# Performance work log

Measured on AMD Instinct MI355X. Metric: run time of the kernel, lower is better.

## Reference

```python
import jax, jax.numpy as jnp
import numpy as np

N_POIS = 100000
N_HYPEREDGES = 50000
NNZ = 1600000
D = 256
NUM_LAYERS = 2
P_DROP = 0.3


def setup_inputs() -> dict:
    key = jax.random.key(0)
    ks = jax.random.split(key, 10)
    scale = 1.0 / (1.0 - P_DROP)
    drop1 = jax.random.bernoulli(ks[4], 1.0 - P_DROP, (NUM_LAYERS, N_POIS, D)).astype(jnp.float32) * scale
    drop2 = jax.random.bernoulli(ks[5], 1.0 - P_DROP, (NUM_LAYERS, N_POIS, D)).astype(jnp.float32) * scale
    return {
        "pois_embs": jax.random.normal(ks[0], (N_POIS, D), dtype=jnp.float32),
        "tar_vals": jax.random.uniform(ks[1], (NNZ,), dtype=jnp.float32),
        "src_vals": jax.random.uniform(ks[2], (NNZ,), dtype=jnp.float32),
        "layer_attention": jnp.ones((NUM_LAYERS + 1,), dtype=jnp.float32),
        "drop1": drop1,
        "drop2": drop2,
        "tar_rows": jax.random.randint(ks[6], (NNZ,), 0, N_HYPEREDGES, dtype=jnp.int32),
        "tar_cols": jax.random.randint(ks[7], (NNZ,), 0, N_POIS, dtype=jnp.int32),
        "src_rows": jax.random.randint(ks[8], (NNZ,), 0, N_POIS, dtype=jnp.int32),
        "src_cols": jax.random.randint(ks[9], (NNZ,), 0, N_HYPEREDGES, dtype=jnp.int32),
    }


def _spmm(rows, cols, vals, dense, num_rows):
    # COO sparse @ dense: gather rows of `dense` by cols, scale, scatter-add by rows
    return jax.ops.segment_sum(vals[:, None] * dense[cols], rows, num_segments=num_rows)


def reference(pois_embs, tar_vals, src_vals, layer_attention, drop1, drop2,
              tar_rows, tar_cols, src_rows, src_cols):
    embs = pois_embs
    layer_outs = [embs]
    for i in range(NUM_LAYERS):
        # msg_tar = HG_poi_tar @ embs  -> [n_hyperedges, d]
        msg_tar = _spmm(tar_rows, tar_cols, tar_vals, embs, N_HYPEREDGES)
        # msg_src = HG_poi_src @ msg_tar -> [n_pois, d]
        msg_src = _spmm(src_rows, src_cols, src_vals, msg_tar, N_POIS)
        msg_src = jax.nn.relu(msg_src) * drop1[i]      # conv-layer dropout
        embs = (msg_src + layer_outs[-1]) * drop2[i]   # residual + F.dropout
        layer_outs.append(embs)
    w = jax.nn.softmax(layer_attention)                # [num_layers+1]
    stacked = jnp.stack(layer_outs)                    # [L+1, n_pois, d]
    return jnp.sum(stacked * w[:, None, None], axis=0)
```

## Files before the change

### kernel.cpp

```cpp
#include <hip/hip_runtime.h>

#define NPOIS 100000
#define NHYP  50000
#define NNZE  1600000
#define DIM   256

#define SH_TAR 6
#define SH_SRC 7
#define NBUCK 782
#define CHUNK 6250

typedef unsigned int uint;

#define DROP_C ((float)(1.0 / (1.0 - 0.3)))

__device__ __forceinline__ uint pack_bf16(float a, float b) {
    uint ua = __float_as_uint(a); ua += 0x7fffu + ((ua >> 16) & 1u);
    uint ub = __float_as_uint(b); ub += 0x7fffu + ((ub >> 16) & 1u);
    return (ua >> 16) | (ub & 0xffff0000u);
}
__device__ __forceinline__ float4 unpack_h(uint2 u) {
    return make_float4(__uint_as_float(u.x << 16), __uint_as_float(u.x & 0xffff0000u),
                       __uint_as_float(u.y << 16), __uint_as_float(u.y & 0xffff0000u));
}

__global__ __launch_bounds__(256) void to_h_kernel(
    const float4* __restrict__ in, uint2* __restrict__ out, int n4)
{
    int stride = gridDim.x * blockDim.x;
    for (int i = blockIdx.x * blockDim.x + threadIdx.x; i < n4; i += stride) {
        float4 x = in[i];
        out[i] = make_uint2(pack_bf16(x.x, x.y), pack_bf16(x.z, x.w));
    }
}

__global__ __launch_bounds__(256) void drop_bits_kernel(
    const float4* __restrict__ d1, const float4* __restrict__ d2,
    uint* __restrict__ o1, uint* __restrict__ o2, int nw)
{
    int t = blockIdx.x * blockDim.x + threadIdx.x;
    if (t >= 2 * nw) return;
    const float4* src = (t < nw) ? d1 : d2;
    uint* dst = (t < nw) ? o1 : o2;
    int w = (t < nw) ? t : t - nw;
    uint m = 0;
#pragma unroll
    for (int q = 0; q < 8; ++q) {
        float4 v = src[(size_t)w * 8 + q];
        m |= (v.x != 0.f ? 1u : 0u) << (4 * q);
        m |= (v.y != 0.f ? 2u : 0u) << (4 * q);
        m |= (v.z != 0.f ? 4u : 0u) << (4 * q);
        m |= (v.w != 0.f ? 8u : 0u) << (4 * q);
    }
    dst[w] = m;
}


__global__ __launch_bounds__(256) void hist_coarse(
    const int* __restrict__ tr, const int* __restrict__ sr,
    int* __restrict__ c_tar, int* __restrict__ c_src, int nnz)
{
    __shared__ int lt[NBUCK], ls[NBUCK];
    int t = threadIdx.x;
    int s = blockIdx.x * CHUNK, e = min(s + CHUNK, nnz);
    for (int i = t; i < NBUCK; i += 256) { lt[i] = 0; ls[i] = 0; }
    __syncthreads();
    for (int i = s + t; i < e; i += 256) {
        atomicAdd(&lt[tr[i] >> SH_TAR], 1);
        atomicAdd(&ls[sr[i] >> SH_SRC], 1);
    }
    __syncthreads();
    for (int i = t; i < NBUCK; i += 256) {
        if (lt[i]) atomicAdd(&c_tar[i], lt[i]);
        if (ls[i]) atomicAdd(&c_src[i], ls[i]);
    }
}

__global__ __launch_bounds__(256) void scan_offsets(
    const int* __restrict__ c_tar, const int* __restrict__ c_src,
    int* __restrict__ off_tar, int* __restrict__ tl_tar,
    int* __restrict__ off_src, int* __restrict__ tl_src)
{
    __shared__ int lds[256];
    int t = threadIdx.x;
    for (int sel = 0; sel < 2; ++sel) {
        const int* c = sel ? c_src : c_tar;
        int* off = sel ? off_src : off_tar;
        int* tl  = sel ? tl_src : tl_tar;
        int carry = 0;
        for (int base = 0; base < NBUCK; base += 256) {
            int i = base + t;
            int v = (i < NBUCK) ? c[i] : 0;
            lds[t] = v;
            __syncthreads();
            for (int o = 1; o < 256; o <<= 1) {
                int x = (t >= o) ? lds[t - o] : 0;
                __syncthreads();
                lds[t] += x;
                __syncthreads();
            }
            int excl = carry + lds[t] - v;
            if (i < NBUCK) { off[i] = excl; tl[i] = excl; }
            carry += lds[255];
            __syncthreads();
        }
        if (t == 0) off[NBUCK] = carry;
        __syncthreads();
    }
}

__global__ __launch_bounds__(256) void csr_stage(
    const int* __restrict__ tar_rows, const int* __restrict__ tar_cols,
    const float* __restrict__ tar_vals,
    const int* __restrict__ src_rows, const int* __restrict__ src_cols,
    const float* __restrict__ src_vals,
    int* __restrict__ tl_tar, uint2* __restrict__ stag_tar,
    int* __restrict__ tl_src, uint2* __restrict__ stag_src, int nnz)
{
    __shared__ int lh[NBUCK];
    __shared__ int lbase[NBUCK];
    int t = threadIdx.x;
    bool is_src = blockIdx.x >= 256;
    int blk = is_src ? blockIdx.x - 256 : blockIdx.x;
    const int* rows = is_src ? src_rows : tar_rows;
    const int* cols = is_src ? src_cols : tar_cols;
    const float* vals = is_src ? src_vals : tar_vals;
    int* tails = is_src ? tl_src : tl_tar;
    uint2* stag = is_src ? stag_src : stag_tar;
    const int SH = is_src ? SH_SRC : SH_TAR;

    int s = blk * CHUNK, e = min(s + CHUNK, nnz);
    for (int i = t; i < NBUCK; i += 256) lh[i] = 0;
    __syncthreads();
    for (int i = s + t; i < e; i += 256) atomicAdd(&lh[rows[i] >> SH], 1);
    __syncthreads();
    for (int i = t; i < NBUCK; i += 256) {
        int c = lh[i];
        lbase[i] = c ? atomicAdd(&tails[i], c) : 0;
        lh[i] = 0;
    }
    __syncthreads();
    for (int i = s + t; i < e; i += 256) {
        int r = rows[i];
        int b = r >> SH;
        int pos = lbase[b] + atomicAdd(&lh[b], 1);
        uint uv = __float_as_uint(vals[i]);
        uv += 0x7fffu + ((uv >> 16) & 1u);
        stag[pos] = make_uint2((uint)r, ((uint)cols[i] << 15) | ((uv >> 16) & 0x7fffu));
    }
}

__global__ __launch_bounds__(256) void csr_finalize(
    const uint2* __restrict__ stag_tar, const int* __restrict__ off_tar,
    int* __restrict__ rp_tar, uint* __restrict__ ep_tar,
    const uint2* __restrict__ stag_src, const int* __restrict__ off_src,
    int* __restrict__ rp_src, uint* __restrict__ ep_src, int nnz)
{
    __shared__ uint2 recs[4096];
    __shared__ int lhist[128];
    __shared__ int lbase[129];
    bool is_src = blockIdx.x >= NBUCK;
    int b = is_src ? blockIdx.x - NBUCK : blockIdx.x;
    const uint2* stag = is_src ? stag_src : stag_tar;
    const int* off = is_src ? off_src : off_tar;
    int* rp = is_src ? rp_src : rp_tar;
    uint* ep = is_src ? ep_src : ep_tar;
    const int SH = is_src ? SH_SRC : SH_TAR;
    const int RPB = 1 << SH;
    const int nrows = is_src ? NPOIS : NHYP;
    int t = threadIdx.x;
    int base = off[b];
    int n = off[b + 1] - base;
    int r0 = b << SH;

    for (int i = t; i < RPB; i += 256) lhist[i] = 0;
    __syncthreads();

    bool fit = (n <= 4096);
    for (int i = t; i < n; i += 256) {
        uint2 rec = stag[base + i];
        if (fit) recs[i] = rec;
        atomicAdd(&lhist[(int)rec.x - r0], 1);
    }
    __syncthreads();
    if (t == 0) {
        int run = 0;
        for (int i = 0; i < RPB; ++i) { lbase[i] = run; run += lhist[i]; }
        lbase[RPB] = run;
    }
    __syncthreads();
    for (int i = t; i < RPB; i += 256) {
        int rg = r0 + i;
        if (rg < nrows) rp[rg] = base + lbase[i];
    }
    if (b == 0 && t == 0) rp[nrows] = nnz;
    for (int i = t; i < RPB; i += 256) lhist[i] = 0;
    __syncthreads();
    for (int i = t; i < n; i += 256) {
        uint2 rec = fit ? recs[i] : stag[base + i];
        int rl = (int)rec.x - r0;
        int slot = lbase[rl] + atomicAdd(&lhist[rl], 1);
        ep[base + slot] = rec.y;
    }
}

#define GCH 8

__device__ __forceinline__ float4 gather_h(
    const int* __restrict__ rp, const uint* __restrict__ ep,
    const uint2* __restrict__ dh, int row, int lane)
{
    int s = rp[row], e = rp[row + 1];
    float4 acc = {0.f, 0.f, 0.f, 0.f};
    for (int k = s; k < e; k += GCH) {
        uint ev[GCH];
#pragma unroll
        for (int j = 0; j < GCH; ++j)
            ev[j] = (k + j < e) ? ep[k + j] : 0u;
        uint2 x[GCH];
#pragma unroll
        for (int j = 0; j < GCH; ++j)
            x[j] = dh[(size_t)(ev[j] >> 15) * (DIM / 4) + lane];
#pragma unroll
        for (int j = 0; j < GCH; ++j) {
            float vv = __uint_as_float((ev[j] & 0x7fffu) << 16);
            acc.x += vv * __uint_as_float(x[j].x << 16);
            acc.y += vv * __uint_as_float(x[j].x & 0xffff0000u);
            acc.z += vv * __uint_as_float(x[j].y << 16);
            acc.w += vv * __uint_as_float(x[j].y & 0xffff0000u);
        }
    }
    return acc;
}

__device__ __forceinline__ float4 gather_f(
    const int* __restrict__ rp, const uint* __restrict__ ep,
    const float4* __restrict__ d4, int row, int lane)
{
    int s = rp[row], e = rp[row + 1];
    float4 acc = {0.f, 0.f, 0.f, 0.f};
    for (int k = s; k < e; k += GCH) {
        uint ev[GCH];
#pragma unroll
        for (int j = 0; j < GCH; ++j)
            ev[j] = (k + j < e) ? ep[k + j] : 0u;
        float4 x[GCH];
#pragma unroll
        for (int j = 0; j < GCH; ++j)
            x[j] = d4[(size_t)(ev[j] >> 15) * (DIM / 4) + lane];
#pragma unroll
        for (int j = 0; j < GCH; ++j) {
            float vv = __uint_as_float((ev[j] & 0x7fffu) << 16);
            acc.x += vv * x[j].x;
            acc.y += vv * x[j].y;
            acc.z += vv * x[j].z;
            acc.w += vv * x[j].w;
        }
    }
    return acc;
}

__device__ __forceinline__ float4 drop4(const uint* __restrict__ bm, int row, int lane)
{
    uint m = bm[(size_t)row * 8 + (lane >> 3)] >> ((lane & 7) * 4);
    return make_float4((m & 1u) ? DROP_C : 0.f, (m & 2u) ? DROP_C : 0.f,
                       (m & 4u) ? DROP_C : 0.f, (m & 8u) ? DROP_C : 0.f);
}

template <bool BF16D>
__global__ __launch_bounds__(256) void spmm_to_h(
    const int* __restrict__ rp, const uint* __restrict__ ep,
    const void* __restrict__ dense, uint2* __restrict__ out_h, int nrows)
{
    int wid  = (blockIdx.x * blockDim.x + threadIdx.x) >> 6;
    int lane = threadIdx.x & 63;
    if (wid >= nrows) return;
    int row = __builtin_amdgcn_readfirstlane(wid);
    float4 a = BF16D ? gather_h(rp, ep, (const uint2*)dense, row, lane)
                     : gather_f(rp, ep, (const float4*)dense, row, lane);
    out_h[(size_t)row * (DIM / 4) + lane] = make_uint2(pack_bf16(a.x, a.y), pack_bf16(a.z, a.w));
}

template <bool PH, bool BITS>
__global__ __launch_bounds__(256) void spmm_epi1(
    const int* __restrict__ rp, const uint* __restrict__ ep,
    const uint2* __restrict__ msg_h,
    const uint2* __restrict__ pois_h, const float4* __restrict__ pois_f,
    const float4* __restrict__ d1, const float4* __restrict__ d2,
    const uint* __restrict__ bm1, const uint* __restrict__ bm2,
    uint2* __restrict__ out_h, int nrows)
{
    int wid  = (blockIdx.x * blockDim.x + threadIdx.x) >> 6;
    int lane = threadIdx.x & 63;
    if (wid >= nrows) return;
    int row = __builtin_amdgcn_readfirstlane(wid);
    size_t idx = (size_t)row * (DIM / 4) + lane;
    float4 a, b;
    if (BITS) { a = drop4(bm1, row, lane); b = drop4(bm2, row, lane); }
    else      { a = d1[idx]; b = d2[idx]; }
    float4 p = PH ? unpack_h(pois_h[idx]) : pois_f[idx];
    float4 m = gather_h(rp, ep, msg_h, row, lane);
    float4 r;
    r.x = (fmaxf(m.x, 0.f) * a.x + p.x) * b.x;
    r.y = (fmaxf(m.y, 0.f) * a.y + p.y) * b.y;
    r.z = (fmaxf(m.z, 0.f) * a.z + p.z) * b.z;
    r.w = (fmaxf(m.w, 0.f) * a.w + p.w) * b.w;
    out_h[idx] = make_uint2(pack_bf16(r.x, r.y), pack_bf16(r.z, r.w));
}

template <bool PH, bool BITS>
__global__ __launch_bounds__(256) void spmm_final(
    const int* __restrict__ rp, const uint* __restrict__ ep,
    const uint2* __restrict__ msg_h,
    const uint2* __restrict__ pois_h, const float4* __restrict__ pois_f,
    const uint2* __restrict__ embs1_h,
    const float4* __restrict__ d1, const float4* __restrict__ d2,
    const uint* __restrict__ bm1, const uint* __restrict__ bm2,
    const float* __restrict__ attn, float4* __restrict__ out, int nrows)
{
    int wid  = (blockIdx.x * blockDim.x + threadIdx.x) >> 6;
    int lane = threadIdx.x & 63;
    if (wid >= nrows) return;
    int row = __builtin_amdgcn_readfirstlane(wid);

    float a0 = attn[0], a1 = attn[1], a2 = attn[2];
    float mx = fmaxf(a0, fmaxf(a1, a2));
    float e0 = __expf(a0 - mx), e1 = __expf(a1 - mx), e2 = __expf(a2 - mx);
    float inv = 1.f / (e0 + e1 + e2);
    float w0 = e0 * inv, w1 = e1 * inv, w2 = e2 * inv;

    size_t idx = (size_t)row * (DIM / 4) + lane;
    float4 a, b;
    if (BITS) { a = drop4(bm1, row, lane); b = drop4(bm2, row, lane); }
    else      { a = d1[idx]; b = d2[idx]; }
    float4 p0 = PH ? unpack_h(pois_h[idx]) : pois_f[idx];
    float4 p1 = unpack_h(embs1_h[idx]);
    float4 m = gather_h(rp, ep, msg_h, row, lane);
    float4 r;
    r.x = w0 * p0.x + w1 * p1.x + w2 * ((fmaxf(m.x, 0.f) * a.x + p1.x) * b.x);
    r.y = w0 * p0.y + w1 * p1.y + w2 * ((fmaxf(m.y, 0.f) * a.y + p1.y) * b.y);
    r.z = w0 * p0.z + w1 * p1.z + w2 * ((fmaxf(m.z, 0.f) * a.z + p1.z) * b.z);
    r.w = w0 * p0.w + w1 * p1.w + w2 * ((fmaxf(m.w, 0.f) * a.w + p1.w) * b.w);
    out[idx] = r;
}

extern "C" void kernel_launch(void* const* d_in, const int* in_sizes, int n_in,
                              void* d_out, int out_size, void* d_ws, size_t ws_size,
                              hipStream_t stream)
{
    const float* pois     = (const float*)d_in[0];
    const float* tar_vals = (const float*)d_in[1];
    const float* src_vals = (const float*)d_in[2];
    const float* attn     = (const float*)d_in[3];
    const float* drop1    = (const float*)d_in[4];
    const float* drop2    = (const float*)d_in[5];
    const int*   tar_rows = (const int*)d_in[6];
    const int*   tar_cols = (const int*)d_in[7];
    const int*   src_rows = (const int*)d_in[8];
    const int*   src_cols = (const int*)d_in[9];
    float* out = (float*)d_out;

    const size_t ptn = (size_t)NPOIS * DIM;

    char* p = (char*)d_ws;
    uint* ep_tar   = (uint*)p;              p += (size_t)NNZE * 4;
    uint* ep_src   = (uint*)p;              p += (size_t)NNZE * 4;
    int*  rp_tar   = (int*)p;               p += 200064;
    int*  rp_src   = (int*)p;               p += 400064;
    int*  misc     = (int*)p;               p += 32768;
    uint2* msg_h   = (uint2*)p;             p += (size_t)NHYP * DIM * 2;
    uint2* embs1_h = (uint2*)p;             p += (size_t)NPOIS * DIM * 2;

    const size_t bits_words = (size_t)2 * NPOIS * 8;
    uint* bits1 = (uint*)p;
    uint* bits2 = bits1 + bits_words;       p += 2 * bits_words * 4;
    size_t bits_need = (size_t)(p - (char*)d_ws);
    bool have_bits = ws_size >= bits_need;

    uint2* pois_h  = (uint2*)p;
    bool full = ws_size >= bits_need + ptn * 2;

    int* cntc_tar = misc;
    int* off_tar  = cntc_tar + NBUCK;
    int* tl_tar   = off_tar + NBUCK + 1;
    int* cntc_src = tl_tar + NBUCK;
    int* off_src  = cntc_src + NBUCK;
    int* tl_src   = off_src + NBUCK + 1;

    uint2* stag_tar = (uint2*)msg_h;
    uint2* stag_src = stag_tar + NNZE;

    const int BLK = 256;

    if (full)
        to_h_kernel<<<(int)(ptn / 4 + BLK - 1) / BLK, BLK, 0, stream>>>(
            (const float4*)pois, pois_h, (int)(ptn / 4));

    if (have_bits) {
        int nw = (int)(2 * ptn / 32);
        drop_bits_kernel<<<(2 * nw + BLK - 1) / BLK, BLK, 0, stream>>>(
            (const float4*)drop1, (const float4*)drop2, bits1, bits2, nw);
    }

    hipMemsetAsync(misc, 0, 32768, stream);
    hist_coarse<<<256, BLK, 0, stream>>>(tar_rows, src_rows, cntc_tar, cntc_src, NNZE);
    scan_offsets<<<1, BLK, 0, stream>>>(cntc_tar, cntc_src, off_tar, tl_tar, off_src, tl_src);
    csr_stage<<<512, BLK, 0, stream>>>(
        tar_rows, tar_cols, tar_vals, src_rows, src_cols, src_vals,
        tl_tar, stag_tar, tl_src, stag_src, NNZE);
    csr_finalize<<<2 * NBUCK, BLK, 0, stream>>>(
        stag_tar, off_tar, rp_tar, ep_tar,
        stag_src, off_src, rp_src, ep_src, NNZE);

    const int gb_hyp = NHYP / 4;
    const int gb_poi = NPOIS / 4;

    const float4* d1_l0 = (const float4*)drop1;
    const float4* d2_l0 = (const float4*)drop2;
    const float4* d1_l1 = (const float4*)(drop1 + ptn);
    const float4* d2_l1 = (const float4*)(drop2 + ptn);
    const uint* b1_l0 = bits1;
    const uint* b2_l0 = bits2;
    const uint* b1_l1 = bits1 + (size_t)NPOIS * 8;
    const uint* b2_l1 = bits2 + (size_t)NPOIS * 8;

    if (full)
        spmm_to_h<true><<<gb_hyp, BLK, 0, stream>>>(rp_tar, ep_tar, pois_h, msg_h, NHYP);
    else
        spmm_to_h<false><<<gb_hyp, BLK, 0, stream>>>(rp_tar, ep_tar, pois, msg_h, NHYP);

    if (full && have_bits)
        spmm_epi1<true, true><<<gb_poi, BLK, 0, stream>>>(
            rp_src, ep_src, msg_h, pois_h, (const float4*)pois,
            d1_l0, d2_l0, b1_l0, b2_l0, embs1_h, NPOIS);
    else if (full)
        spmm_epi1<true, false><<<gb_poi, BLK, 0, stream>>>(
            rp_src, ep_src, msg_h, pois_h, (const float4*)pois,
            d1_l0, d2_l0, b1_l0, b2_l0, embs1_h, NPOIS);
    else if (have_bits)
        spmm_epi1<false, true><<<gb_poi, BLK, 0, stream>>>(
            rp_src, ep_src, msg_h, pois_h, (const float4*)pois,
            d1_l0, d2_l0, b1_l0, b2_l0, embs1_h, NPOIS);
    else
        spmm_epi1<false, false><<<gb_poi, BLK, 0, stream>>>(
            rp_src, ep_src, msg_h, pois_h, (const float4*)pois,
            d1_l0, d2_l0, b1_l0, b2_l0, embs1_h, NPOIS);

    spmm_to_h<true><<<gb_hyp, BLK, 0, stream>>>(rp_tar, ep_tar, embs1_h, msg_h, NHYP);

    if (full && have_bits)
        spmm_final<true, true><<<gb_poi, BLK, 0, stream>>>(
            rp_src, ep_src, msg_h, pois_h, (const float4*)pois, embs1_h,
            d1_l1, d2_l1, b1_l1, b2_l1, attn, (float4*)out, NPOIS);
    else if (full)
        spmm_final<true, false><<<gb_poi, BLK, 0, stream>>>(
            rp_src, ep_src, msg_h, pois_h, (const float4*)pois, embs1_h,
            d1_l1, d2_l1, b1_l1, b2_l1, attn, (float4*)out, NPOIS);
    else if (have_bits)
        spmm_final<false, true><<<gb_poi, BLK, 0, stream>>>(
            rp_src, ep_src, msg_h, pois_h, (const float4*)pois, embs1_h,
            d1_l1, d2_l1, b1_l1, b2_l1, attn, (float4*)out, NPOIS);
    else
        spmm_final<false, false><<<gb_poi, BLK, 0, stream>>>(
            rp_src, ep_src, msg_h, pois_h, (const float4*)pois, embs1_h,
            d1_l1, d2_l1, b1_l1, b2_l1, attn, (float4*)out, NPOIS);
}
```

Measured before the change: 1.184 ms.

## Fuse whole pipeline into one cooperative persistent kernel with grid syncs

Replaces the sequence of separate kernel launches (bf16 conversion, dropout bit packing, CSR build via bucketed histogram/scatter, two SpMM layers with fused epilogues) with a single cooperative persistent kernel that separates phases with grid-wide syncs. The aim is to remove per-launch overhead and gaps between kernels. In exchange, the grid is capped at occupancy times 256 blocks, and the sort phases lose the earlier per-bucket LDS record caching. Grid syncs also cost time, and serial single-block scans now stall the whole grid. The old multi-kernel path is kept as a fallback if the cooperative launch fails.

```diff
diff --git a/kernel.cpp b/kernel.cpp
--- a/kernel.cpp
+++ b/kernel.cpp
@@ -1,4 +1,7 @@
 #include <hip/hip_runtime.h>
+#include <hip/hip_cooperative_groups.h>
+
+namespace cg = cooperative_groups;
 
 #define NPOIS 100000
 #define NHYP  50000
@@ -14,6 +17,19 @@
 
 #define DROP_C ((float)(1.0 / (1.0 - 0.3)))
 
+#define OFF_EPT   0
+#define OFF_EPS   6400000
+#define OFF_RPT   12800000
+#define OFF_RPS   13000064
+#define OFF_MISC  13400128
+#define OFF_MSG   13432896
+#define OFF_EMB   39032896
+#define OFF_BITS1 90232896
+#define OFF_BITS2 96632896
+#define OFF_POISH 103032896
+#define NEED_BITS 103032896
+#define NEED_FULL 154232896
+
 __device__ __forceinline__ uint pack_bf16(float a, float b) {
     uint ua = __float_as_uint(a); ua += 0x7fffu + ((ua >> 16) & 1u);
     uint ub = __float_as_uint(b); ub += 0x7fffu + ((ub >> 16) & 1u);
@@ -22,6 +38,331 @@
 __device__ __forceinline__ float4 unpack_h(uint2 u) {
     return make_float4(__uint_as_float(u.x << 16), __uint_as_float(u.x & 0xffff0000u),
                        __uint_as_float(u.y << 16), __uint_as_float(u.y & 0xffff0000u));
+}
+
+#define GCH 8
+
+__device__ __forceinline__ float4 gather_h(
+    const int* rp, const uint* ep, const uint2* dh, int row, int lane)
+{
+    int s = rp[row], e = rp[row + 1];
+    float4 acc = {0.f, 0.f, 0.f, 0.f};
+    for (int k = s; k < e; k += GCH) {
+        uint ev[GCH];
+#pragma unroll
+        for (int j = 0; j < GCH; ++j)
+            ev[j] = (k + j < e) ? ep[k + j] : 0u;
+        uint2 x[GCH];
+#pragma unroll
+        for (int j = 0; j < GCH; ++j)
+            x[j] = dh[(size_t)(ev[j] >> 15) * (DIM / 4) + lane];
+#pragma unroll
+        for (int j = 0; j < GCH; ++j) {
+            float vv = __uint_as_float((ev[j] & 0x7fffu) << 16);
+            acc.x += vv * __uint_as_float(x[j].x << 16);
+            acc.y += vv * __uint_as_float(x[j].x & 0xffff0000u);
+            acc.z += vv * __uint_as_float(x[j].y << 16);
+            acc.w += vv * __uint_as_float(x[j].y & 0xffff0000u);
+        }
+    }
+    return acc;
+}
+
+__device__ __forceinline__ float4 gather_f(
+    const int* rp, const uint* ep, const float4* d4, int row, int lane)
+{
+    int s = rp[row], e = rp[row + 1];
+    float4 acc = {0.f, 0.f, 0.f, 0.f};
+    for (int k = s; k < e; k += GCH) {
+        uint ev[GCH];
+#pragma unroll
+        for (int j = 0; j < GCH; ++j)
+            ev[j] = (k + j < e) ? ep[k + j] : 0u;
+        float4 x[GCH];
+#pragma unroll
+        for (int j = 0; j < GCH; ++j)
+            x[j] = d4[(size_t)(ev[j] >> 15) * (DIM / 4) + lane];
+#pragma unroll
+        for (int j = 0; j < GCH; ++j) {
+            float vv = __uint_as_float((ev[j] & 0x7fffu) << 16);
+            acc.x += vv * x[j].x;
+            acc.y += vv * x[j].y;
+            acc.z += vv * x[j].z;
+            acc.w += vv * x[j].w;
+        }
+    }
+    return acc;
+}
+
+__device__ __forceinline__ float4 drop4(const uint* bm, int row, int lane)
+{
+    uint m = bm[(size_t)row * 8 + (lane >> 3)] >> ((lane & 7) * 4);
+    return make_float4((m & 1u) ? DROP_C : 0.f, (m & 2u) ? DROP_C : 0.f,
+                       (m & 4u) ? DROP_C : 0.f, (m & 8u) ? DROP_C : 0.f);
+}
+
+__global__ __launch_bounds__(256) void mega(
+    const float* pois, const float* tar_vals, const float* src_vals,
+    const float* attn, const float* drop1, const float* drop2,
+    const int* tar_rows, const int* tar_cols,
+    const int* src_rows, const int* src_cols,
+    float4* out, char* ws, int full, int have_bits)
+{
+    cg::grid_group grid = cg::this_grid();
+
+    uint*  ep_tar  = (uint*)(ws + OFF_EPT);
+    uint*  ep_src  = (uint*)(ws + OFF_EPS);
+    int*   rp_tar  = (int*)(ws + OFF_RPT);
+    int*   rp_src  = (int*)(ws + OFF_RPS);
+    int*   misc    = (int*)(ws + OFF_MISC);
+    uint2* msg_h   = (uint2*)(ws + OFF_MSG);
+    uint2* embs1_h = (uint2*)(ws + OFF_EMB);
+    uint*  bits1   = (uint*)(ws + OFF_BITS1);
+    uint*  bits2   = (uint*)(ws + OFF_BITS2);
+    uint2* pois_h  = (uint2*)(ws + OFF_POISH);
+
+    int* cntc_tar = misc;
+    int* off_tar  = cntc_tar + NBUCK;
+    int* tl_tar   = off_tar + NBUCK + 1;
+    int* cntc_src = tl_tar + NBUCK;
+    int* off_src  = cntc_src + NBUCK;
+    int* tl_src   = off_src + NBUCK + 1;
+
+    uint2* stag_tar = (uint2*)msg_h;
+    uint2* stag_src = stag_tar + NNZE;
+
+    __shared__ int lds_a[NBUCK];
+    __shared__ int lds_b[NBUCK];
+
+    const int B    = gridDim.x;
+    const int t    = threadIdx.x;
+    const int tid  = blockIdx.x * 256 + t;
+    const int nthr = B * 256;
+    const int lane = t & 63;
+    const int w0   = tid >> 6;
+    const int wstr = nthr >> 6;
+
+    for (int i = tid; i < 8192; i += nthr) misc[i] = 0;
+    if (full) {
+        const float4* pin = (const float4*)pois;
+        for (int i = tid; i < NPOIS * DIM / 4; i += nthr) {
+            float4 x = pin[i];
+            pois_h[i] = make_uint2(pack_bf16(x.x, x.y), pack_bf16(x.z, x.w));
+        }
+    }
+    if (have_bits) {
+        const float4* s1 = (const float4*)drop1;
+        const float4* s2 = (const float4*)drop2;
+        for (int w = tid; w < 1600000; w += nthr) {
+            uint m1 = 0, m2 = 0;
+#pragma unroll
+            for (int q = 0; q < 8; ++q) {
+                float4 v = s1[(size_t)w * 8 + q];
+                m1 |= (v.x != 0.f ? 1u : 0u) << (4 * q);
+                m1 |= (v.y != 0.f ? 2u : 0u) << (4 * q);
+                m1 |= (v.z != 0.f ? 4u : 0u) << (4 * q);
+                m1 |= (v.w != 0.f ? 8u : 0u) << (4 * q);
+                float4 u = s2[(size_t)w * 8 + q];
+                m2 |= (u.x != 0.f ? 1u : 0u) << (4 * q);
+                m2 |= (u.y != 0.f ? 2u : 0u) << (4 * q);
+                m2 |= (u.z != 0.f ? 4u : 0u) << (4 * q);
+                m2 |= (u.w != 0.f ? 8u : 0u) << (4 * q);
+            }
+            bits1[w] = m1; bits2[w] = m2;
+        }
+    }
+    grid.sync();
+
+    {
+        int per = (NNZE + B - 1) / B;
+        int s = blockIdx.x * per, e = min(s + per, NNZE);
+        for (int i = t; i < NBUCK; i += 256) { lds_a[i] = 0; lds_b[i] = 0; }
+        __syncthreads();
+        for (int i = s + t; i < e; i += 256) {
+            atomicAdd(&lds_a[tar_rows[i] >> SH_TAR], 1);
+            atomicAdd(&lds_b[src_rows[i] >> SH_SRC], 1);
+        }
+        __syncthreads();
+        for (int i = t; i < NBUCK; i += 256) {
+            if (lds_a[i]) atomicAdd(&cntc_tar[i], lds_a[i]);
+            if (lds_b[i]) atomicAdd(&cntc_src[i], lds_b[i]);
+        }
+    }
+    grid.sync();
+
+    if (blockIdx.x == 0) {
+        for (int sel = 0; sel < 2; ++sel) {
+            const int* c = sel ? cntc_src : cntc_tar;
+            int* off = sel ? off_src : off_tar;
+            int* tl  = sel ? tl_src : tl_tar;
+            int carry = 0;
+            for (int base = 0; base < NBUCK; base += 256) {
+                int i = base + t;
+                int v = (i < NBUCK) ? c[i] : 0;
+                lds_a[t] = v;
+                __syncthreads();
+                for (int o = 1; o < 256; o <<= 1) {
+                    int x = (t >= o) ? lds_a[t - o] : 0;
+                    __syncthreads();
+                    lds_a[t] += x;
+                    __syncthreads();
+                }
+                int excl = carry + lds_a[t] - v;
+                if (i < NBUCK) { off[i] = excl; tl[i] = excl; }
+                carry += lds_a[255];
+                __syncthreads();
+            }
+            if (t == 0) off[NBUCK] = carry;
+            __syncthreads();
+        }
+    }
+    grid.sync();
+
+    for (int c = blockIdx.x; c < 512; c += B) {
+        bool is_src = c >= 256;
+        int blk = c & 255;
+        const int* rows = is_src ? src_rows : tar_rows;
+        const int* cols = is_src ? src_cols : tar_cols;
+        const float* vals = is_src ? src_vals : tar_vals;
+        int* tails = is_src ? tl_src : tl_tar;
+        uint2* stag = is_src ? stag_src : stag_tar;
+        const int SH = is_src ? SH_SRC : SH_TAR;
+        int s = blk * CHUNK, e = min(s + CHUNK, NNZE);
+        for (int i = t; i < NBUCK; i += 256) lds_a[i] = 0;
+        __syncthreads();
+        for (int i = s + t; i < e; i += 256) atomicAdd(&lds_a[rows[i] >> SH], 1);
+        __syncthreads();
+        for (int i = t; i < NBUCK; i += 256) {
+            int cc = lds_a[i];
+            lds_b[i] = cc ? atomicAdd(&tails[i], cc) : 0;
+            lds_a[i] = 0;
+        }
+        __syncthreads();
+        for (int i = s + t; i < e; i += 256) {
+            int r = rows[i];
+            int b = r >> SH;
+            int pos = lds_b[b] + atomicAdd(&lds_a[b], 1);
+            uint uv = __float_as_uint(vals[i]);
+            uv += 0x7fffu + ((uv >> 16) & 1u);
+            stag[pos] = make_uint2((uint)r, ((uint)cols[i] << 15) | ((uv >> 16) & 0x7fffu));
+        }
+        __syncthreads();
+    }
+    grid.sync();
+
+    for (int c = blockIdx.x; c < 2 * NBUCK; c += B) {
+        bool is_src = c >= NBUCK;
+        int b = is_src ? c - NBUCK : c;
+        const uint2* stag = is_src ? stag_src : stag_tar;
+        const int* off = is_src ? off_src : off_tar;
+        int* rp = is_src ? rp_src : rp_tar;
+        uint* ep = is_src ? ep_src : ep_tar;
+        const int SH = is_src ? SH_SRC : SH_TAR;
+        const int RPB = 1 << SH;
+        const int nrows = is_src ? NPOIS : NHYP;
+        int base = off[b];
+        int n = off[b + 1] - base;
+        int r0 = b << SH;
+        for (int i = t; i < RPB; i += 256) lds_a[i] = 0;
+        __syncthreads();
+        for (int i = t; i < n; i += 256)
+            atomicAdd(&lds_a[(int)stag[base + i].x - r0], 1);
+        __syncthreads();
+        if (t == 0) {
+            int run = 0;
+            for (int i = 0; i < RPB; ++i) { lds_b[i] = run; run += lds_a[i]; }
+        }
+        __syncthreads();
+        for (int i = t; i < RPB; i += 256) {
+            int rg = r0 + i;
+            if (rg < nrows) rp[rg] = base + lds_b[i];
+        }
+        for (int i = t; i < RPB; i += 256) lds_a[i] = 0;
+        __syncthreads();
+        for (int i = t; i < n; i += 256) {
+            uint2 rec = stag[base + i];
+            int rl = (int)rec.x - r0;
+            int slot = lds_b[rl] + atomicAdd(&lds_a[rl], 1);
+            ep[base + slot] = rec.y;
+        }
+        __syncthreads();
+    }
+    if (blockIdx.x == 0 && t == 0) { rp_tar[NHYP] = NNZE; rp_src[NPOIS] = NNZE; }
+    grid.sync();
+
+    if (full) {
+        for (int r = w0; r < NHYP; r += wstr) {
+            int row = __builtin_amdgcn_readfirstlane(r);
+            float4 a = gather_h(rp_tar, ep_tar, pois_h, row, lane);
+            msg_h[(size_t)row * (DIM / 4) + lane] =
+                make_uint2(pack_bf16(a.x, a.y), pack_bf16(a.z, a.w));
+        }
+    } else {
+        for (int r = w0; r < NHYP; r += wstr) {
+            int row = __builtin_amdgcn_readfirstlane(r);
+            float4 a = gather_f(rp_tar, ep_tar, (const float4*)pois, row, lane);
+            msg_h[(size_t)row * (DIM / 4) + lane] =
+                make_uint2(pack_bf16(a.x, a.y), pack_bf16(a.z, a.w));
+        }
+    }
+    grid.sync();
+
+    {
+        const float4* d1 = (const float4*)drop1;
+        const float4* d2 = (const float4*)drop2;
+        for (int r = w0; r < NPOIS; r += wstr) {
+            int row = __builtin_amdgcn_readfirstlane(r);
+            size_t idx = (size_t)row * (DIM / 4) + lane;
+            float4 a, b;
+            if (have_bits) { a = drop4(bits1, row, lane); b = drop4(bits2, row, lane); }
+            else           { a = d1[idx]; b = d2[idx]; }
+            float4 p = full ? unpack_h(pois_h[idx]) : ((const float4*)pois)[idx];
+            float4 m = gather_h(rp_src, ep_src, msg_h, row, lane);
+            float4 o;
+            o.x = (fmaxf(m.x, 0.f) * a.x + p.x) * b.x;
+            o.y = (fmaxf(m.y, 0.f) * a.y + p.y) * b.y;
+            o.z = (fmaxf(m.z, 0.f) * a.z + p.z) * b.z;
+            o.w = (fmaxf(m.w, 0.f) * a.w + p.w) * b.w;
+            embs1_h[idx] = make_uint2(pack_bf16(o.x, o.y), pack_bf16(o.z, o.w));
+        }
+    }
+    grid.sync();
+
+    for (int r = w0; r < NHYP; r += wstr) {
+        int row = __builtin_amdgcn_readfirstlane(r);
+        float4 a = gather_h(rp_tar, ep_tar, embs1_h, row, lane);
+        msg_h[(size_t)row * (DIM / 4) + lane] =
+            make_uint2(pack_bf16(a.x, a.y), pack_bf16(a.z, a.w));
+    }
+    grid.sync();
+
+    {
+        float t0 = attn[0], t1 = attn[1], t2 = attn[2];
+        float mx = fmaxf(t0, fmaxf(t1, t2));
+        float e0 = __expf(t0 - mx), e1 = __expf(t1 - mx), e2 = __expf(t2 - mx);
+        float inv = 1.f / (e0 + e1 + e2);
+        float wt0 = e0 * inv, wt1 = e1 * inv, wt2 = e2 * inv;
+        const float4* d1 = (const float4*)(drop1 + (size_t)NPOIS * DIM);
+        const float4* d2 = (const float4*)(drop2 + (size_t)NPOIS * DIM);
+        const uint* b1 = bits1 + (size_t)NPOIS * 8;
+        const uint* b2 = bits2 + (size_t)NPOIS * 8;
+        for (int r = w0; r < NPOIS; r += wstr) {
+            int row = __builtin_amdgcn_readfirstlane(r);
+            size_t idx = (size_t)row * (DIM / 4) + lane;
+            float4 a, b;
+            if (have_bits) { a = drop4(b1, row, lane); b = drop4(b2, row, lane); }
+            else           { a = d1[idx]; b = d2[idx]; }
+            float4 p0 = full ? unpack_h(pois_h[idx]) : ((const float4*)pois)[idx];
+            float4 p1 = unpack_h(embs1_h[idx]);
+            float4 m = gather_h(rp_src, ep_src, msg_h, row, lane);
+            float4 o;
+            o.x = wt0 * p0.x + wt1 * p1.x + wt2 * ((fmaxf(m.x, 0.f) * a.x + p1.x) * b.x);
+            o.y = wt0 * p0.y + wt1 * p1.y + wt2 * ((fmaxf(m.y, 0.f) * a.y + p1.y) * b.y);
+            o.z = wt0 * p0.z + wt1 * p1.z + wt2 * ((fmaxf(m.z, 0.f) * a.z + p1.z) * b.z);
+            o.w = wt0 * p0.w + wt1 * p1.w + wt2 * ((fmaxf(m.w, 0.f) * a.w + p1.w) * b.w);
+            out[idx] = o;
+        }
+    }
 }
 
 __global__ __launch_bounds__(256) void to_h_kernel(
@@ -54,7 +395,6 @@
     }
     dst[w] = m;
 }
-
 
 __global__ __launch_bounds__(256) void hist_coarse(
     const int* __restrict__ tr, const int* __restrict__ sr,
@@ -175,7 +515,6 @@
 
     for (int i = t; i < RPB; i += 256) lhist[i] = 0;
     __syncthreads();
-
     bool fit = (n <= 4096);
     for (int i = t; i < n; i += 256) {
         uint2 rec = stag[base + i];
@@ -202,69 +541,6 @@
         int slot = lbase[rl] + atomicAdd(&lhist[rl], 1);
         ep[base + slot] = rec.y;
     }
-}
-
-#define GCH 8
-
-__device__ __forceinline__ float4 gather_h(
-    const int* __restrict__ rp, const uint* __restrict__ ep,
-    const uint2* __restrict__ dh, int row, int lane)
-{
-    int s = rp[row], e = rp[row + 1];
-    float4 acc = {0.f, 0.f, 0.f, 0.f};
-    for (int k = s; k < e; k += GCH) {
-        uint ev[GCH];
-#pragma unroll
-        for (int j = 0; j < GCH; ++j)
-            ev[j] = (k + j < e) ? ep[k + j] : 0u;
-        uint2 x[GCH];
-#pragma unroll
-        for (int j = 0; j < GCH; ++j)
-            x[j] = dh[(size_t)(ev[j] >> 15) * (DIM / 4) + lane];
-#pragma unroll
-        for (int j = 0; j < GCH; ++j) {
-            float vv = __uint_as_float((ev[j] & 0x7fffu) << 16);
-            acc.x += vv * __uint_as_float(x[j].x << 16);
-            acc.y += vv * __uint_as_float(x[j].x & 0xffff0000u);
-            acc.z += vv * __uint_as_float(x[j].y << 16);
-            acc.w += vv * __uint_as_float(x[j].y & 0xffff0000u);
-        }
-    }
-    return acc;
-}
-
-__device__ __forceinline__ float4 gather_f(
-    const int* __restrict__ rp, const uint* __restrict__ ep,
-    const float4* __restrict__ d4, int row, int lane)
-{
-    int s = rp[row], e = rp[row + 1];
-    float4 acc = {0.f, 0.f, 0.f, 0.f};
-    for (int k = s; k < e; k += GCH) {
-        uint ev[GCH];
-#pragma unroll
-        for (int j = 0; j < GCH; ++j)
-            ev[j] = (k + j < e) ? ep[k + j] : 0u;
-        float4 x[GCH];
-#pragma unroll
-        for (int j = 0; j < GCH; ++j)
-            x[j] = d4[(size_t)(ev[j] >> 15) * (DIM / 4) + lane];
-#pragma unroll
-        for (int j = 0; j < GCH; ++j) {
-            float vv = __uint_as_float((ev[j] & 0x7fffu) << 16);
-            acc.x += vv * x[j].x;
-            acc.y += vv * x[j].y;
-            acc.z += vv * x[j].z;
-            acc.w += vv * x[j].w;
-        }
-    }
-    return acc;
-}
-
-__device__ __forceinline__ float4 drop4(const uint* __restrict__ bm, int row, int lane)
-{
-    uint m = bm[(size_t)row * 8 + (lane >> 3)] >> ((lane & 7) * 4);
-    return make_float4((m & 1u) ? DROP_C : 0.f, (m & 2u) ? DROP_C : 0.f,
-                       (m & 4u) ? DROP_C : 0.f, (m & 8u) ? DROP_C : 0.f);
 }
 
 template <bool BF16D>
@@ -358,27 +634,48 @@
     const int*   tar_cols = (const int*)d_in[7];
     const int*   src_rows = (const int*)d_in[8];
     const int*   src_cols = (const int*)d_in[9];
-    float* out = (float*)d_out;
+    float4* out = (float4*)d_out;
+    char* ws = (char*)d_ws;
 
     const size_t ptn = (size_t)NPOIS * DIM;
-
-    char* p = (char*)d_ws;
-    uint* ep_tar   = (uint*)p;              p += (size_t)NNZE * 4;
-    uint* ep_src   = (uint*)p;              p += (size_t)NNZE * 4;
-    int*  rp_tar   = (int*)p;               p += 200064;
-    int*  rp_src   = (int*)p;               p += 400064;
-    int*  misc     = (int*)p;               p += 32768;
-    uint2* msg_h   = (uint2*)p;             p += (size_t)NHYP * DIM * 2;
-    uint2* embs1_h = (uint2*)p;             p += (size_t)NPOIS * DIM * 2;
-
-    const size_t bits_words = (size_t)2 * NPOIS * 8;
-    uint* bits1 = (uint*)p;
-    uint* bits2 = bits1 + bits_words;       p += 2 * bits_words * 4;
-    size_t bits_need = (size_t)(p - (char*)d_ws);
-    bool have_bits = ws_size >= bits_need;
-
-    uint2* pois_h  = (uint2*)p;
-    bool full = ws_size >= bits_need + ptn * 2;
+    int have_bits = ws_size >= (size_t)NEED_BITS ? 1 : 0;
+    int full      = ws_size >= (size_t)NEED_FULL ? 1 : 0;
+
+    static int nblk = -1;
+    if (nblk < 0) {
+        int occ = 0;
+        hipError_t oe = hipOccupancyMaxActiveBlocksPerMultiprocessor(
+            &occ, (const void*)mega, 256, 0);
+        if (oe != hipSuccess || occ < 1) nblk = 0;
+        else {
+            nblk = occ * 256;
+            if (nblk > 2048) nblk = 2048;
+        }
+    }
+
+    bool done = false;
+    if (nblk > 0) {
+        void* args[] = {
+            (void*)&pois, (void*)&tar_vals, (void*)&src_vals, (void*)&attn,
+            (void*)&drop1, (void*)&drop2, (void*)&tar_rows, (void*)&tar_cols,
+            (void*)&src_rows, (void*)&src_cols, (void*)&out, (void*)&ws,
+            (void*)&full, (void*)&have_bits };
+        hipError_t err = hipLaunchCooperativeKernel(
+            (const void*)mega, dim3(nblk), dim3(256), args, 0, stream);
+        if (err == hipSuccess) done = true;
+    }
+    if (done) return;
+
+    uint*  ep_tar  = (uint*)(ws + OFF_EPT);
+    uint*  ep_src  = (uint*)(ws + OFF_EPS);
+    int*   rp_tar  = (int*)(ws + OFF_RPT);
+    int*   rp_src  = (int*)(ws + OFF_RPS);
+    int*   misc    = (int*)(ws + OFF_MISC);
+    uint2* msg_h   = (uint2*)(ws + OFF_MSG);
+    uint2* embs1_h = (uint2*)(ws + OFF_EMB);
+    uint*  bits1   = (uint*)(ws + OFF_BITS1);
+    uint*  bits2   = (uint*)(ws + OFF_BITS2);
+    uint2* pois_h  = (uint2*)(ws + OFF_POISH);
 
     int* cntc_tar = misc;
     int* off_tar  = cntc_tar + NBUCK;
@@ -451,17 +748,17 @@
     if (full && have_bits)
         spmm_final<true, true><<<gb_poi, BLK, 0, stream>>>(
             rp_src, ep_src, msg_h, pois_h, (const float4*)pois, embs1_h,
-            d1_l1, d2_l1, b1_l1, b2_l1, attn, (float4*)out, NPOIS);
+            d1_l1, d2_l1, b1_l1, b2_l1, attn, out, NPOIS);
     else if (full)
         spmm_final<true, false><<<gb_poi, BLK, 0, stream>>>(
             rp_src, ep_src, msg_h, pois_h, (const float4*)pois, embs1_h,
-            d1_l1, d2_l1, b1_l1, b2_l1, attn, (float4*)out, NPOIS);
+            d1_l1, d2_l1, b1_l1, b2_l1, attn, out, NPOIS);
     else if (have_bits)
         spmm_final<false, true><<<gb_poi, BLK, 0, stream>>>(
             rp_src, ep_src, msg_h, pois_h, (const float4*)pois, embs1_h,
-            d1_l1, d2_l1, b1_l1, b2_l1, attn, (float4*)out, NPOIS);
+            d1_l1, d2_l1, b1_l1, b2_l1, attn, out, NPOIS);
     else
         spmm_final<false, false><<<gb_poi, BLK, 0, stream>>>(
             rp_src, ep_src, msg_h, pois_h, (const float4*)pois, embs1_h,
-            d1_l1, d2_l1, b1_l1, b2_l1, attn, (float4*)out, NPOIS);
-}
+            d1_l1, d2_l1, b1_l1, b2_l1, attn, out, NPOIS);
+}
```

Result: slower. 2.215 ms (+87.0%).
